# Performance work log

Measured on AMD Instinct MI355X. Metric: run time of the kernel, lower is better.

## Reference

```python
import jax, jax.numpy as jnp
import numpy as np

D_MODEL = 1024
NUM_HEADS = 16
HEAD_DIM = D_MODEL // NUM_HEADS


def setup_inputs() -> dict:
    key = jax.random.key(0)
    k_x, k_qkv, k_o = jax.random.split(key, 3)
    B, L = 2, 2048
    x = jax.random.normal(k_x, (B, L, D_MODEL), dtype=jnp.float32)
    # torch Linear weight [out, in]; y = x @ W.T. Scale ~ kaiming-uniform-ish.
    s = 1.0 / np.sqrt(D_MODEL)
    W_qkv = jax.random.uniform(k_qkv, (3 * D_MODEL, D_MODEL), dtype=jnp.float32, minval=-s, maxval=s)
    W_o = jax.random.uniform(k_o, (D_MODEL, D_MODEL), dtype=jnp.float32, minval=-s, maxval=s)
    return {"x": x, "W_qkv": W_qkv, "W_o": W_o}


def reference(x, W_qkv, W_o):
    B, L, D = x.shape
    H, dk = NUM_HEADS, HEAD_DIM
    qkv = (x @ W_qkv.T).reshape(B, L, 3, H, dk)
    q = qkv[:, :, 0].transpose(0, 2, 1, 3)  # [B,H,L,dk]
    k = qkv[:, :, 1].transpose(0, 2, 1, 3)
    v = qkv[:, :, 2].transpose(0, 2, 1, 3)
    scale = 1.0 / np.sqrt(dk).astype(np.float32)
    attn = jnp.einsum('bhqd,bhkd->bhqk', q, k) * scale  # [B,H,L,L]
    causal = jnp.tril(jnp.ones((L, L), dtype=bool))
    attn = jnp.where(causal, attn, -jnp.inf)
    attn = jax.nn.softmax(attn, axis=-1)
    y = jnp.einsum('bhqk,bhkd->bhqd', attn, v)  # [B,H,L,dk]
    y = y.transpose(0, 2, 1, 3).reshape(B, L, D)
    return y @ W_o.T
```

## Files before the change

kernel.cpp:

```cpp
#include <hip/hip_runtime.h>

typedef unsigned short u16;
typedef unsigned int   u32;

typedef __attribute__((ext_vector_type(4))) float  f32x4;
typedef __attribute__((ext_vector_type(8))) __bf16 bf16x8;

#define B_  2
#define L_  2048
#define H_  16

__device__ static inline u16 f2bf(float f) {
  u32 u = __builtin_bit_cast(u32, f);
  u32 r = u + 0x7fffu + ((u >> 16) & 1u);
  return (u16)(r >> 16);
}
__device__ static inline u32 pack2(float a, float b) {
  return (u32)f2bf(a) | ((u32)f2bf(b) << 16);
}

__device__ static inline void gload_lds16(const u16* g, u16* lds) {
  __builtin_amdgcn_global_load_lds((__attribute__((address_space(1))) void*)(g),
                                   (__attribute__((address_space(3))) void*)(lds),
                                   16, 0, 0);
}

__global__ __launch_bounds__(256) void cvt3_kernel(
    const float4* __restrict__ a, uint2* __restrict__ ao, int na,
    const float4* __restrict__ b, uint2* __restrict__ bo, int nb,
    const float4* __restrict__ c, uint2* __restrict__ co, int nc)
{
  const int step = gridDim.x * 256;
  for (int i = blockIdx.x * 256 + threadIdx.x; i < na; i += step) {
    float4 f = a[i];
    ao[i] = make_uint2(pack2(f.x, f.y), pack2(f.z, f.w));
  }
  for (int i = blockIdx.x * 256 + threadIdx.x; i < nb; i += step) {
    float4 f = b[i];
    bo[i] = make_uint2(pack2(f.x, f.y), pack2(f.z, f.w));
  }
  for (int i = blockIdx.x * 256 + threadIdx.x; i < nc; i += step) {
    float4 f = c[i];
    co[i] = make_uint2(pack2(f.x, f.y), pack2(f.z, f.w));
  }
}

template <bool OUT_F32>
__global__ __launch_bounds__(256) void gemm_bt_kernel(
    const u16* __restrict__ A, const u16* __restrict__ Bt, void* __restrict__ Cv,
    const int K, const int N)
{
  __shared__ __attribute__((aligned(16))) u16 Al[128 * 64];
  __shared__ __attribute__((aligned(16))) u16 Bl[128 * 64];

  const int tid  = threadIdx.x;
  const int w    = tid >> 6;
  const int lane = tid & 63;
  const int m0 = blockIdx.y * 128;
  const int n0 = blockIdx.x * 128;
  const int mo = (w >> 1) * 64;
  const int no = (w & 1) * 64;

  const int srow = w * 32 + (lane >> 3);
  const int scol = (((lane & 7) ^ ((lane >> 3) & 7)) * 8);

  const f32x4 zero = {0.f, 0.f, 0.f, 0.f};
  f32x4 acc[4][4];
  #pragma unroll
  for (int i = 0; i < 4; ++i)
    #pragma unroll
    for (int j = 0; j < 4; ++j) acc[i][j] = zero;

  const int frow = lane & 15;
  const int fg   = lane >> 4;

  for (int k0 = 0; k0 < K; k0 += 64) {
    __syncthreads();
    #pragma unroll
    for (int inst = 0; inst < 4; ++inst) {
      const int r = srow + inst * 8;
      gload_lds16(A  + (size_t)(m0 + r) * K + k0 + scol, &Al[(w * 32 + inst * 8) * 64]);
      gload_lds16(Bt + (size_t)(n0 + r) * K + k0 + scol, &Bl[(w * 32 + inst * 8) * 64]);
    }
    __syncthreads();
    #pragma unroll
    for (int ks = 0; ks < 2; ++ks) {
      const int fco = ((ks * 4 + fg) ^ (frow & 7)) * 8;
      bf16x8 af[4], bfr[4];
      #pragma unroll
      for (int i = 0; i < 4; ++i)
        af[i] = *(const bf16x8*)&Al[(mo + i * 16 + frow) * 64 + fco];
      #pragma unroll
      for (int j = 0; j < 4; ++j)
        bfr[j] = *(const bf16x8*)&Bl[(no + j * 16 + frow) * 64 + fco];
      #pragma unroll
      for (int i = 0; i < 4; ++i)
        #pragma unroll
        for (int j = 0; j < 4; ++j)
          acc[i][j] = __builtin_amdgcn_mfma_f32_16x16x32_bf16(af[i], bfr[j], acc[i][j], 0, 0, 0);
    }
  }

  const int crow0 = m0 + mo + (lane >> 4) * 4;
  const int ccol0 = n0 + no + (lane & 15);
  #pragma unroll
  for (int i = 0; i < 4; ++i)
    #pragma unroll
    for (int j = 0; j < 4; ++j)
      #pragma unroll
      for (int r = 0; r < 4; ++r) {
        const size_t idx = (size_t)(crow0 + i * 16 + r) * N + (ccol0 + j * 16);
        if (OUT_F32) ((float*)Cv)[idx] = acc[i][j][r];
        else         ((u16*)Cv)[idx]   = f2bf(acc[i][j][r]);
      }
}

__global__ __launch_bounds__(256) void attn_mfma_kernel(const u16* __restrict__ qkv,
                                                        u16* __restrict__ y)
{
  __shared__ __attribute__((aligned(16))) u16 Kt[2][64 * 64];
  __shared__ __attribute__((aligned(16))) u32 Vtd[2][64 * 32];
  __shared__ __attribute__((aligned(16))) u32 PTd[4][16 * 32];

  const int tid  = threadIdx.x;
  const int w    = tid >> 6;
  const int lane = tid & 63;
  const int fr   = lane & 15;
  const int fg   = lane >> 4;
  const int bh   = blockIdx.x;
  const int pi   = blockIdx.y;
  const int bb   = bh >> 4;
  const int hh   = bh & 15;
  const size_t rb = (size_t)bb * L_;

  const int kkp = lane & 31;
  const int dc  = 2 * w + (lane >> 5);

  const int ksr = w * 16 + (lane >> 3);
  const int ksc = (((lane & 7) ^ ((lane >> 3) & 7)) * 8);
  const int kco0 = ((fg) ^ (fr & 7)) * 8;
  const int kco1 = ((4 + fg) ^ (fr & 7)) * 8;

  const int cro0 = 4 * ((fg) ^ (fr & 7));
  const int cro1 = 4 * ((4 + fg) ^ (fr & 7));
  const int pwo = 4 * (fr & 7);

  const f32x4 zero = {0.f, 0.f, 0.f, 0.f};

  for (int pass = 0; pass < 2; ++pass) {
    const int qt = pass ? (31 - pi) : pi;
    const int q0 = qt * 64;
    const int qw = q0 + w * 16;

    const bf16x8 qf0 = *(const bf16x8*)(qkv + (rb + qw + fr) * 3072 + hh * 64 + fg * 8);
    const bf16x8 qf1 = *(const bf16x8*)(qkv + (rb + qw + fr) * 3072 + hh * 64 + 32 + fg * 8);

    f32x4 oacc[4];
    #pragma unroll
    for (int mt = 0; mt < 4; ++mt) oacc[mt] = zero;
    float lsum = 0.f;

    __syncthreads();
    #pragma unroll
    for (int inst = 0; inst < 2; ++inst)
      gload_lds16(qkv + (rb + ksr + inst * 8) * 3072 + 1024 + hh * 64 + ksc,
                  &Kt[0][(w * 16 + inst * 8) * 64]);
    {
      const u16* vp = qkv + (rb + 2 * kkp) * 3072 + 2048 + hh * 64 + dc * 8;
      uint4 va = *(const uint4*)vp;
      uint4 vb = *(const uint4*)(vp + 3072);
      u16 a16[8], b16[8];
      *(uint4*)a16 = va; *(uint4*)b16 = vb;
      #pragma unroll
      for (int i = 0; i < 8; ++i)
        Vtd[0][(dc * 8 + i) * 32 + 4 * ((kkp >> 2) ^ i) + (kkp & 3)] =
            (u32)a16[i] | ((u32)b16[i] << 16);
    }

    int cur = 0;
    for (int kt = 0; kt <= q0; kt += 64) {
      __syncthreads();

      const bool havenext = (kt + 64 <= q0);
      uint4 va, vb;
      if (havenext) {
        #pragma unroll
        for (int inst = 0; inst < 2; ++inst)
          gload_lds16(qkv + (rb + kt + 64 + ksr + inst * 8) * 3072 + 1024 + hh * 64 + ksc,
                      &Kt[cur ^ 1][(w * 16 + inst * 8) * 64]);
        const u16* vp = qkv + (rb + kt + 64 + 2 * kkp) * 3072 + 2048 + hh * 64 + dc * 8;
        va = *(const uint4*)vp;
        vb = *(const uint4*)(vp + 3072);
      }

      f32x4 sacc[4];
      #pragma unroll
      for (int nt = 0; nt < 4; ++nt) sacc[nt] = zero;
      #pragma unroll
      for (int nt = 0; nt < 4; ++nt) {
        bf16x8 kf0 = *(const bf16x8*)&Kt[cur][(nt * 16 + fr) * 64 + kco0];
        sacc[nt] = __builtin_amdgcn_mfma_f32_16x16x32_bf16(kf0, qf0, sacc[nt], 0, 0, 0);
        bf16x8 kf1 = *(const bf16x8*)&Kt[cur][(nt * 16 + fr) * 64 + kco1];
        sacc[nt] = __builtin_amdgcn_mfma_f32_16x16x32_bf16(kf1, qf1, sacc[nt], 0, 0, 0);
      }

      if (kt == q0) {
        #pragma unroll
        for (int nt = 0; nt < 4; ++nt) {
          float p[4];
          #pragma unroll
          for (int r = 0; r < 4; ++r) {
            p[r] = (nt * 16 + 4 * fg + r > w * 16 + fr)
                       ? 0.f : __expf(sacc[nt][r] * 0.125f);
            lsum += p[r];
          }
          *(uint2*)&PTd[w][fr * 32 + ((8 * nt + 2 * fg) ^ pwo)] =
              make_uint2(pack2(p[0], p[1]), pack2(p[2], p[3]));
        }
      } else {
        #pragma unroll
        for (int nt = 0; nt < 4; ++nt) {
          float p[4];
          #pragma unroll
          for (int r = 0; r < 4; ++r) {
            p[r] = __expf(sacc[nt][r] * 0.125f);
            lsum += p[r];
          }
          *(uint2*)&PTd[w][fr * 32 + ((8 * nt + 2 * fg) ^ pwo)] =
              make_uint2(pack2(p[0], p[1]), pack2(p[2], p[3]));
        }
      }

      #pragma unroll
      for (int ks = 0; ks < 2; ++ks) {
        bf16x8 pf = *(const bf16x8*)&PTd[w][fr * 32 + (ks ? cro1 : cro0)];
        #pragma unroll
        for (int mt = 0; mt < 4; ++mt) {
          bf16x8 vf = *(const bf16x8*)&Vtd[cur][(mt * 16 + fr) * 32 + (ks ? cro1 : cro0)];
          oacc[mt] = __builtin_amdgcn_mfma_f32_16x16x32_bf16(vf, pf, oacc[mt], 0, 0, 0);
        }
      }

      if (havenext) {
        u16 a16[8], b16[8];
        *(uint4*)a16 = va; *(uint4*)b16 = vb;
        #pragma unroll
        for (int i = 0; i < 8; ++i)
          Vtd[cur ^ 1][(dc * 8 + i) * 32 + 4 * ((kkp >> 2) ^ i) + (kkp & 3)] =
              (u32)a16[i] | ((u32)b16[i] << 16);
      }
      cur ^= 1;
    }

    lsum += __shfl_xor(lsum, 16);
    lsum += __shfl_xor(lsum, 32);
    const float inv = 1.f / lsum;

    u16* yp = y + (rb + qw + fr) * 1024 + hh * 64 + 4 * fg;
    #pragma unroll
    for (int mt = 0; mt < 4; ++mt)
      *(uint2*)(yp + mt * 16) = make_uint2(pack2(oacc[mt][0] * inv, oacc[mt][1] * inv),
                                           pack2(oacc[mt][2] * inv, oacc[mt][3] * inv));
  }
}

extern "C" void kernel_launch(void* const* d_in, const int* in_sizes, int n_in,
                              void* d_out, int out_size, void* d_ws, size_t ws_size,
                              hipStream_t stream)
{
  const float* x    = (const float*)d_in[0];
  const float* Wqkv = (const float*)d_in[1];
  const float* Wo   = (const float*)d_in[2];
  float* out = (float*)d_out;

  u16* xb    = (u16*)d_ws;
  u16* Wqkvb = xb    + (size_t)4096 * 1024;
  u16* Wob   = Wqkvb + (size_t)3072 * 1024;
  u16* qkv   = Wob   + (size_t)1024 * 1024;
  u16* y     = qkv   + (size_t)4096 * 3072;

  cvt3_kernel<<<dim3(2048), dim3(256), 0, stream>>>(
      (const float4*)x,    (uint2*)xb,    4096 * 1024 / 4,
      (const float4*)Wqkv, (uint2*)Wqkvb, 3072 * 1024 / 4,
      (const float4*)Wo,   (uint2*)Wob,   1024 * 1024 / 4);

  gemm_bt_kernel<false><<<dim3(3072 / 128, 4096 / 128), dim3(256), 0, stream>>>(
      xb, Wqkvb, qkv, 1024, 3072);
  attn_mfma_kernel<<<dim3(B_ * H_, 16), dim3(256), 0, stream>>>(qkv, y);
  gemm_bt_kernel<true><<<dim3(1024 / 128, 4096 / 128), dim3(256), 0, stream>>>(
      y, Wob, out, 1024, 1024);
}
```

Baseline: 184.8 us.

## Split KV range across two wave groups per attention block and merge via LDS

The attention block grows to 512 threads. Two 256-thread groups each process half of the causal key tiles for the same query tile, each with its own double-buffered K/V in LDS. Group 1 writes its partial output and row sums to LDS, and group 0 combines them and writes the result. This shortens the serial KV loop per block and raises the wave count, at the cost of more LDS per block, extra barriers and a merge step.

```diff
diff --git a/kernel.cpp b/kernel.cpp
--- a/kernel.cpp
+++ b/kernel.cpp
@@ -115,15 +115,14 @@
       }
 }
 
-__global__ __launch_bounds__(256) void attn_mfma_kernel(const u16* __restrict__ qkv,
+__global__ __launch_bounds__(512) void attn_mfma_kernel(const u16* __restrict__ qkv,
                                                         u16* __restrict__ y)
 {
-  __shared__ __attribute__((aligned(16))) u16 Kt[2][64 * 64];
-  __shared__ __attribute__((aligned(16))) u32 Vtd[2][64 * 32];
-  __shared__ __attribute__((aligned(16))) u32 PTd[4][16 * 32];
+  __shared__ __attribute__((aligned(16))) unsigned char smem[81920];
 
   const int tid  = threadIdx.x;
-  const int w    = tid >> 6;
+  const int g    = tid >> 8;
+  const int w    = (tid >> 6) & 3;
   const int lane = tid & 63;
   const int fr   = lane & 15;
   const int fg   = lane >> 4;
@@ -133,6 +132,12 @@
   const int hh   = bh & 15;
   const size_t rb = (size_t)bb * L_;
 
+  u16* Kt   = (u16*)(smem + g * 40960);
+  u32* Vtd  = (u32*)(smem + g * 40960 + 16384);
+  u32* PTd  = (u32*)(smem + g * 40960 + 32768) + w * 512;
+  float* Ocmb = (float*)(smem + 40960);
+  float* Lcmb = (float*)(smem + 40960 + 17408);
+
   const int kkp = lane & 31;
   const int dc  = 2 * w + (lane >> 5);
 
@@ -143,7 +148,7 @@
 
   const int cro0 = 4 * ((fg) ^ (fr & 7));
   const int cro1 = 4 * ((4 + fg) ^ (fr & 7));
-  const int pwo = 4 * (fr & 7);
+  const int pwo  = 4 * (fr & 7);
 
   const f32x4 zero = {0.f, 0.f, 0.f, 0.f};
 
@@ -151,6 +156,11 @@
     const int qt = pass ? (31 - pi) : pi;
     const int q0 = qt * 64;
     const int qw = q0 + w * 16;
+    const int n  = qt + 1;
+    const int c0 = (n + 1) >> 1;
+    const int myCnt  = g ? (n - c0) : c0;
+    const int myBase = g ? c0 : 0;
+    const int phases = c0;
 
     const bf16x8 qf0 = *(const bf16x8*)(qkv + (rb + qw + fr) * 3072 + hh * 64 + fg * 8);
     const bf16x8 qf1 = *(const bf16x8*)(qkv + (rb + qw + fr) * 3072 + hh * 64 + 32 + fg * 8);
@@ -161,83 +171,88 @@
     float lsum = 0.f;
 
     __syncthreads();
-    #pragma unroll
-    for (int inst = 0; inst < 2; ++inst)
-      gload_lds16(qkv + (rb + ksr + inst * 8) * 3072 + 1024 + hh * 64 + ksc,
-                  &Kt[0][(w * 16 + inst * 8) * 64]);
-    {
-      const u16* vp = qkv + (rb + 2 * kkp) * 3072 + 2048 + hh * 64 + dc * 8;
+    if (myCnt > 0) {
+      const int kt = myBase * 64;
+      #pragma unroll
+      for (int inst = 0; inst < 2; ++inst)
+        gload_lds16(qkv + (rb + kt + ksr + inst * 8) * 3072 + 1024 + hh * 64 + ksc,
+                    &Kt[(w * 16 + inst * 8) * 64]);
+      const u16* vp = qkv + (rb + kt + 2 * kkp) * 3072 + 2048 + hh * 64 + dc * 8;
       uint4 va = *(const uint4*)vp;
       uint4 vb = *(const uint4*)(vp + 3072);
       u16 a16[8], b16[8];
       *(uint4*)a16 = va; *(uint4*)b16 = vb;
       #pragma unroll
       for (int i = 0; i < 8; ++i)
-        Vtd[0][(dc * 8 + i) * 32 + 4 * ((kkp >> 2) ^ i) + (kkp & 3)] =
+        Vtd[(dc * 8 + i) * 32 + 4 * ((kkp >> 2) ^ i) + (kkp & 3)] =
             (u32)a16[i] | ((u32)b16[i] << 16);
     }
 
     int cur = 0;
-    for (int kt = 0; kt <= q0; kt += 64) {
+    for (int it = 0; it < phases; ++it) {
       __syncthreads();
 
-      const bool havenext = (kt + 64 <= q0);
+      const int  kt       = (myBase + it) * 64;
+      const bool active   = it < myCnt;
+      const bool havenext = (it + 1) < myCnt;
       uint4 va, vb;
       if (havenext) {
         #pragma unroll
         for (int inst = 0; inst < 2; ++inst)
           gload_lds16(qkv + (rb + kt + 64 + ksr + inst * 8) * 3072 + 1024 + hh * 64 + ksc,
-                      &Kt[cur ^ 1][(w * 16 + inst * 8) * 64]);
+                      &Kt[(cur ^ 1) * 4096 + (w * 16 + inst * 8) * 64]);
         const u16* vp = qkv + (rb + kt + 64 + 2 * kkp) * 3072 + 2048 + hh * 64 + dc * 8;
         va = *(const uint4*)vp;
         vb = *(const uint4*)(vp + 3072);
       }
 
-      f32x4 sacc[4];
-      #pragma unroll
-      for (int nt = 0; nt < 4; ++nt) sacc[nt] = zero;
-      #pragma unroll
-      for (int nt = 0; nt < 4; ++nt) {
-        bf16x8 kf0 = *(const bf16x8*)&Kt[cur][(nt * 16 + fr) * 64 + kco0];
-        sacc[nt] = __builtin_amdgcn_mfma_f32_16x16x32_bf16(kf0, qf0, sacc[nt], 0, 0, 0);
-        bf16x8 kf1 = *(const bf16x8*)&Kt[cur][(nt * 16 + fr) * 64 + kco1];
-        sacc[nt] = __builtin_amdgcn_mfma_f32_16x16x32_bf16(kf1, qf1, sacc[nt], 0, 0, 0);
-      }
-
-      if (kt == q0) {
+      if (active) {
+        f32x4 sacc[4];
+        #pragma unroll
+        for (int nt = 0; nt < 4; ++nt) sacc[nt] = zero;
         #pragma unroll
         for (int nt = 0; nt < 4; ++nt) {
-          float p[4];
+          bf16x8 kf0 = *(const bf16x8*)&Kt[cur * 4096 + (nt * 16 + fr) * 64 + kco0];
+          sacc[nt] = __builtin_amdgcn_mfma_f32_16x16x32_bf16(kf0, qf0, sacc[nt], 0, 0, 0);
+          bf16x8 kf1 = *(const bf16x8*)&Kt[cur * 4096 + (nt * 16 + fr) * 64 + kco1];
+          sacc[nt] = __builtin_amdgcn_mfma_f32_16x16x32_bf16(kf1, qf1, sacc[nt], 0, 0, 0);
+        }
+
+        if (kt == q0) {
           #pragma unroll
-          for (int r = 0; r < 4; ++r) {
-            p[r] = (nt * 16 + 4 * fg + r > w * 16 + fr)
-                       ? 0.f : __expf(sacc[nt][r] * 0.125f);
-            lsum += p[r];
+          for (int nt = 0; nt < 4; ++nt) {
+            float p[4];
+            #pragma unroll
+            for (int r = 0; r < 4; ++r) {
+              p[r] = (nt * 16 + 4 * fg + r > w * 16 + fr)
+                         ? 0.f : __expf(sacc[nt][r] * 0.125f);
+              lsum += p[r];
+            }
+            *(uint2*)&PTd[fr * 32 + ((8 * nt + 2 * fg) ^ pwo)] =
+                make_uint2(pack2(p[0], p[1]), pack2(p[2], p[3]));
           }
-          *(uint2*)&PTd[w][fr * 32 + ((8 * nt + 2 * fg) ^ pwo)] =
-              make_uint2(pack2(p[0], p[1]), pack2(p[2], p[3]));
+        } else {
+          #pragma unroll
+          for (int nt = 0; nt < 4; ++nt) {
+            float p[4];
+            #pragma unroll
+            for (int r = 0; r < 4; ++r) {
+              p[r] = __expf(sacc[nt][r] * 0.125f);
+              lsum += p[r];
+            }
+            *(uint2*)&PTd[fr * 32 + ((8 * nt + 2 * fg) ^ pwo)] =
+                make_uint2(pack2(p[0], p[1]), pack2(p[2], p[3]));
+          }
         }
-      } else {
-        #pragma unroll
-        for (int nt = 0; nt < 4; ++nt) {
-          float p[4];
+
+        #pragma unroll
+        for (int ks = 0; ks < 2; ++ks) {
+          bf16x8 pf = *(const bf16x8*)&PTd[fr * 32 + (ks ? cro1 : cro0)];
           #pragma unroll
-          for (int r = 0; r < 4; ++r) {
-            p[r] = __expf(sacc[nt][r] * 0.125f);
-            lsum += p[r];
+          for (int mt = 0; mt < 4; ++mt) {
+            bf16x8 vf = *(const bf16x8*)&Vtd[cur * 2048 + (mt * 16 + fr) * 32 + (ks ? cro1 : cro0)];
+            oacc[mt] = __builtin_amdgcn_mfma_f32_16x16x32_bf16(vf, pf, oacc[mt], 0, 0, 0);
           }
-          *(uint2*)&PTd[w][fr * 32 + ((8 * nt + 2 * fg) ^ pwo)] =
-              make_uint2(pack2(p[0], p[1]), pack2(p[2], p[3]));
-        }
-      }
-
-      #pragma unroll
-      for (int ks = 0; ks < 2; ++ks) {
-        bf16x8 pf = *(const bf16x8*)&PTd[w][fr * 32 + (ks ? cro1 : cro0)];
-        #pragma unroll
-        for (int mt = 0; mt < 4; ++mt) {
-          bf16x8 vf = *(const bf16x8*)&Vtd[cur][(mt * 16 + fr) * 32 + (ks ? cro1 : cro0)];
-          oacc[mt] = __builtin_amdgcn_mfma_f32_16x16x32_bf16(vf, pf, oacc[mt], 0, 0, 0);
         }
       }
 
@@ -246,7 +261,7 @@
         *(uint4*)a16 = va; *(uint4*)b16 = vb;
         #pragma unroll
         for (int i = 0; i < 8; ++i)
-          Vtd[cur ^ 1][(dc * 8 + i) * 32 + 4 * ((kkp >> 2) ^ i) + (kkp & 3)] =
+          Vtd[(cur ^ 1) * 2048 + (dc * 8 + i) * 32 + 4 * ((kkp >> 2) ^ i) + (kkp & 3)] =
               (u32)a16[i] | ((u32)b16[i] << 16);
       }
       cur ^= 1;
@@ -254,13 +269,25 @@
 
     lsum += __shfl_xor(lsum, 16);
     lsum += __shfl_xor(lsum, 32);
-    const float inv = 1.f / lsum;
-
-    u16* yp = y + (rb + qw + fr) * 1024 + hh * 64 + 4 * fg;
-    #pragma unroll
-    for (int mt = 0; mt < 4; ++mt)
-      *(uint2*)(yp + mt * 16) = make_uint2(pack2(oacc[mt][0] * inv, oacc[mt][1] * inv),
-                                           pack2(oacc[mt][2] * inv, oacc[mt][3] * inv));
+
+    __syncthreads();
+    if (g == 1) {
+      #pragma unroll
+      for (int mt = 0; mt < 4; ++mt)
+        *(f32x4*)&Ocmb[(w * 16 + fr) * 68 + mt * 16 + 4 * fg] = oacc[mt];
+      if (fg == 0) Lcmb[w * 16 + fr] = lsum;
+    }
+    __syncthreads();
+    if (g == 0) {
+      const float inv = 1.f / (lsum + Lcmb[w * 16 + fr]);
+      u16* yp = y + (rb + qw + fr) * 1024 + hh * 64 + 4 * fg;
+      #pragma unroll
+      for (int mt = 0; mt < 4; ++mt) {
+        f32x4 o = oacc[mt] + *(const f32x4*)&Ocmb[(w * 16 + fr) * 68 + mt * 16 + 4 * fg];
+        *(uint2*)(yp + mt * 16) = make_uint2(pack2(o[0] * inv, o[1] * inv),
+                                             pack2(o[2] * inv, o[3] * inv));
+      }
+    }
   }
 }
 
@@ -286,7 +313,7 @@
 
   gemm_bt_kernel<false><<<dim3(3072 / 128, 4096 / 128), dim3(256), 0, stream>>>(
       xb, Wqkvb, qkv, 1024, 3072);
-  attn_mfma_kernel<<<dim3(B_ * H_, 16), dim3(256), 0, stream>>>(qkv, y);
+  attn_mfma_kernel<<<dim3(B_ * H_, 16), dim3(512), 0, stream>>>(qkv, y);
   gemm_bt_kernel<true><<<dim3(1024 / 128, 4096 / 128), dim3(256), 0, stream>>>(
       y, Wob, out, 1024, 1024);
 }
```

New measurement: 180.2 us. -2.5%, faster.
